# Performance work log

Measured on AMD Instinct MI355X. Metric: run time of the kernel, lower is better.

The kernel has to match this reference:

```python
import jax, jax.numpy as jnp
import numpy as np

V, E, H = 50000, 300, 128
B, L, QL, NS = 64, 1024, 32, 16
ITERATIONS = 3


def _gru_cell(x, h, w_ih, w_hh, b_ih, b_hh):
    # PyTorch GRUCell math.
    gi = x @ w_ih.T + b_ih
    gh = h @ w_hh.T + b_hh
    i_r, i_z, i_n = jnp.split(gi, 3, axis=-1)
    h_r, h_z, h_n = jnp.split(gh, 3, axis=-1)
    r = jax.nn.sigmoid(i_r + h_r)
    z = jax.nn.sigmoid(i_z + h_z)
    n = jnp.tanh(i_n + r * h_n)
    return (1.0 - z) * n + z * h


def _gru_scan(x, w_ih, w_hh, b_ih, b_hh):
    # x: [B, T, E] -> all hidden states [B, T, H] (nn.GRU, batch_first, h0=0).
    gi = jnp.einsum('bte,ge->btg', x, w_ih) + b_ih  # precompute input gates
    hdim = w_hh.shape[1]

    def step(h, gi_t):
        gh = h @ w_hh.T + b_hh
        i_r, i_z, i_n = jnp.split(gi_t, 3, axis=-1)
        h_r, h_z, h_n = jnp.split(gh, 3, axis=-1)
        r = jax.nn.sigmoid(i_r + h_r)
        z = jax.nn.sigmoid(i_z + h_z)
        n = jnp.tanh(i_n + r * h_n)
        h = (1.0 - z) * n + z * h
        return h, h

    h0 = jnp.zeros((x.shape[0], hdim), x.dtype)
    _, hs = jax.lax.scan(step, h0, jnp.swapaxes(gi, 0, 1))
    return jnp.swapaxes(hs, 0, 1)


def setup_inputs() -> dict:
    key = jax.random.key(0)
    ks = jax.random.split(key, 16)
    x_stories = jax.random.randint(ks[0], (B, L), 1, V)
    # Exactly NS sentence-end marks per story (evenly spaced) -> equal sent counts.
    pos = jnp.arange(1, NS + 1) * (L // NS) - 1
    x_story_masks = jnp.zeros((B, L), bool).at[:, pos].set(True)
    x_questions = jax.random.randint(ks[1], (B, QL), 1, V)
    emb = jax.random.normal(ks[2], (V, E), jnp.float32) * 0.1
    s = float(1.0 / np.sqrt(H))
    u = lambda k, sh: jax.random.uniform(k, sh, jnp.float32, -s, s)
    return {
        'x_stories': x_stories,
        'x_story_masks': x_story_masks,
        'x_questions': x_questions,
        'n_sents': NS,
        'emb': emb,
        'enc_w_ih': u(ks[3], (3 * H, E)),
        'enc_w_hh': u(ks[4], (3 * H, H)),
        'enc_b_ih': u(ks[5], (3 * H,)),
        'enc_b_hh': u(ks[6], (3 * H,)),
        'gate_w': u(ks[7], (1, 4 * H)),
        'gate_b': u(ks[8], (1,)),
        'ep_w_ih': u(ks[9], (3 * H, H)),
        'ep_w_hh': u(ks[10], (3 * H, H)),
        'ep_b_ih': u(ks[11], (3 * H,)),
        'ep_b_hh': u(ks[12], (3 * H,)),
    }


def reference(x_stories, x_story_masks, x_questions, n_sents, emb,
              enc_w_ih, enc_w_hh, enc_b_ih, enc_b_hh,
              gate_w, gate_b, ep_w_ih, ep_w_hh, ep_b_ih, ep_b_hh):
    Bb, Ll = x_stories.shape
    enc_stories = _gru_scan(emb[x_stories], enc_w_ih, enc_w_hh, enc_b_ih, enc_b_hh)  # [B,L,H]
    # Gather the n_sents masked (sentence-end) hidden states per story, in order.
    ar = jnp.arange(Ll)
    sort_key = jnp.where(x_story_masks, ar, Ll + ar)
    idx = jnp.argsort(sort_key, axis=1)[:, :n_sents]  # [B,NS]
    sents = jnp.take_along_axis(enc_stories, idx[:, :, None], axis=1)  # [B,NS,H]
    # Question encoding; pick hidden at the last token before padding.
    q_enc = _gru_scan(emb[x_questions], enc_w_ih, enc_w_hh, enc_b_ih, enc_b_hh)
    next_zero = jnp.concatenate([x_questions[:, 1:] == 0, jnp.ones((Bb, 1), bool)], axis=1)
    qi = jnp.argmax(next_zero, axis=1)
    q_vecs = q_enc[jnp.arange(Bb), qi]  # [B,H]
    q = q_vecs[:, None, :]
    pw1 = sents * q
    d1 = (sents - q) ** 2
    mem = q
    hdim = ep_w_hh.shape[1]
    for _ in range(ITERATIONS):
        pw2 = sents * mem
        d2 = (sents - mem) ** 2
        feats = jnp.concatenate([pw1, pw2, d1, d2], axis=2)  # [B,NS,4H]
        gates = jax.nn.sigmoid(feats @ gate_w.T + gate_b)[..., 0]  # [B,NS]

        def ep_step(h, inp):
            x_t, w_t = inp
            h_new = _gru_cell(x_t, h, ep_w_ih, ep_w_hh, ep_b_ih, ep_b_hh)
            w = w_t[:, None]
            return w * h_new + (1.0 - w) * h, None

        h0 = jnp.zeros((Bb, hdim), sents.dtype)
        ep_state, _ = jax.lax.scan(ep_step, h0, (jnp.swapaxes(sents, 0, 1), gates.T))
        mem = ep_state[:, None, :]
    return q_vecs, ep_state[None], gates
```

## Files before the change

kernel.cpp:

```cpp
#include <hip/hip_runtime.h>
#include <hip/hip_bf16.h>

#define HDIM 128
#define G3 384
#define EDIM 300
#define KP 320
#define ASTRIDE 328
#define BATCH 64
#define LSTO 1024
#define QLEN 32
#define NSENT 16
#define WGB 16
#define HROW 272
#define HBUF (WGB * HROW)

typedef float4 f4;
typedef __attribute__((ext_vector_type(8))) short bf16x8;
typedef __attribute__((ext_vector_type(4))) float f32x4;

__device__ __forceinline__ float sigmf(float x) { return 1.0f / (1.0f + __expf(-x)); }
__device__ __forceinline__ float tanhfast(float x) {
    float e = __expf(-2.0f * x);
    return (1.0f - e) / (1.0f + e);
}
__device__ __forceinline__ float bf2f(unsigned short u) {
    return __uint_as_float(((unsigned)u) << 16);
}
__device__ __forceinline__ unsigned short f2bf_u(float f) {
    union { __hip_bfloat16 b; unsigned short s; } u;
    u.b = __float2bfloat16(f);
    return u.s;
}
__device__ __forceinline__ short f2bf_s(float f) {
    union { __hip_bfloat16 b; short s; } u;
    u.b = __float2bfloat16(f);
    return u.s;
}
__device__ __forceinline__ bf16x8 packrow8(const float* p) {
    bf16x8 v;
#pragma unroll
    for (int i = 0; i < 8; i++) v[i] = f2bf_s(p[i]);
    return v;
}
__device__ __forceinline__ unsigned pack2bf(float a, float b) {
    return ((unsigned)f2bf_u(b) << 16) | (unsigned)f2bf_u(a);
}
__device__ __forceinline__ void barrier_nodrain() {
    asm volatile("" ::: "memory");
    __builtin_amdgcn_s_barrier();
    asm volatile("" ::: "memory");
}
__device__ __forceinline__ void lgkm0() {
    asm volatile("s_waitcnt lgkmcnt(0)" ::: "memory");
    __builtin_amdgcn_sched_barrier(0);
}

__global__ __launch_bounds__(256) void k_w2bf(
    const float* __restrict__ w, __hip_bfloat16* __restrict__ wb, int rows)
{
    int i = blockIdx.x * 256 + threadIdx.x;
    if (i >= rows * KP) return;
    int r = i / KP, k = i - r * KP;
    float v = (k < EDIM) ? w[(size_t)r * EDIM + k] : 0.f;
    wb[i] = __float2bfloat16(v);
}

__global__ __launch_bounds__(512) void k_gi_mfma(
    const int* __restrict__ toks, int nrows,
    const float* __restrict__ emb,
    const __hip_bfloat16* __restrict__ wb, const float* __restrict__ b_ih,
    const float* __restrict__ b_hh,
    __hip_bfloat16* __restrict__ gi)
{
    __shared__ __hip_bfloat16 a_lds[32 * ASTRIDE];
    const int tid = threadIdx.x;
    const int rowbase = blockIdx.x * 32;

    for (int i = tid; i < 32 * KP; i += 512) {
        int r = i / KP, k = i - r * KP;
        int row = rowbase + r;
        float v = 0.f;
        if (k < EDIM) {
            int tok = (row < nrows) ? toks[row] : 0;
            v = emb[(size_t)tok * EDIM + k];
        }
        a_lds[r * ASTRIDE + k] = __float2bfloat16(v);
    }
    __syncthreads();

    const int w8   = tid >> 6;
    const int l    = tid & 63;
    const int coln = l & 15;
    const int kg   = l >> 4;

    int g0 = w8 * 48 + coln, g1 = g0 + 16, g2 = g0 + 32;
    float bias0 = b_ih[g0] + (g0 < 256 ? b_hh[g0] : 0.f);
    float bias1 = b_ih[g1] + (g1 < 256 ? b_hh[g1] : 0.f);
    float bias2 = b_ih[g2] + (g2 < 256 ? b_hh[g2] : 0.f);

    f32x4 acc[2][3];
#pragma unroll
    for (int mt = 0; mt < 2; mt++) {
        acc[mt][0] = f32x4{bias0, bias0, bias0, bias0};
        acc[mt][1] = f32x4{bias1, bias1, bias1, bias1};
        acc[mt][2] = f32x4{bias2, bias2, bias2, bias2};
    }

    const __hip_bfloat16* bbase = wb + (size_t)(w8 * 48 + coln) * KP + kg * 8;
#pragma unroll
    for (int c = 0; c < KP / 32; ++c) {
        bf16x8 A0 = *reinterpret_cast<const bf16x8*>(
            a_lds + (coln) * ASTRIDE + c * 32 + kg * 8);
        bf16x8 A1 = *reinterpret_cast<const bf16x8*>(
            a_lds + (16 + coln) * ASTRIDE + c * 32 + kg * 8);
        bf16x8 B0 = *reinterpret_cast<const bf16x8*>(bbase + 0 * 16 * KP + c * 32);
        bf16x8 B1 = *reinterpret_cast<const bf16x8*>(bbase + 1 * 16 * KP + c * 32);
        bf16x8 B2 = *reinterpret_cast<const bf16x8*>(bbase + 2 * 16 * KP + c * 32);
        acc[0][0] = __builtin_amdgcn_mfma_f32_16x16x32_bf16(A0, B0, acc[0][0], 0, 0, 0);
        acc[1][0] = __builtin_amdgcn_mfma_f32_16x16x32_bf16(A1, B0, acc[1][0], 0, 0, 0);
        acc[0][1] = __builtin_amdgcn_mfma_f32_16x16x32_bf16(A0, B1, acc[0][1], 0, 0, 0);
        acc[1][1] = __builtin_amdgcn_mfma_f32_16x16x32_bf16(A1, B1, acc[1][1], 0, 0, 0);
        acc[0][2] = __builtin_amdgcn_mfma_f32_16x16x32_bf16(A0, B2, acc[0][2], 0, 0, 0);
        acc[1][2] = __builtin_amdgcn_mfma_f32_16x16x32_bf16(A1, B2, acc[1][2], 0, 0, 0);
    }

#pragma unroll
    for (int mt = 0; mt < 2; mt++) {
#pragma unroll
        for (int nt = 0; nt < 3; nt++) {
            int gate = w8 * 48 + nt * 16 + coln;
#pragma unroll
            for (int q = 0; q < 4; q++) {
                int row = rowbase + mt * 16 + kg * 4 + q;
                if (row < nrows)
                    gi[(size_t)row * G3 + gate] = __float2bfloat16(acc[mt][nt][q]);
            }
        }
    }
}

__global__ __launch_bounds__(192) void k_gi_dense(
    const float* __restrict__ x, int nrows,
    const float* __restrict__ w_ih, const float* __restrict__ b_ih,
    const float* __restrict__ b_hh,
    __hip_bfloat16* __restrict__ gi)
{
    __shared__ alignas(16) float a_lds[32 * HDIM];
    int tid = threadIdx.x;
    int rowbase = blockIdx.x * 32;

    for (int i = tid; i < 32 * 32; i += 192) {
        int r = i >> 5, e4 = i & 31;
        int row = rowbase + r;
        f4 v;
        if (row < nrows) v = *reinterpret_cast<const f4*>(x + (size_t)row * HDIM + e4 * 4);
        else { v.x = v.y = v.z = v.w = 0.f; }
        *reinterpret_cast<f4*>(a_lds + r * HDIM + e4 * 4) = v;
    }
    __syncthreads();

    int g0 = tid, g1 = tid + 192;
    const float* w0p = w_ih + (size_t)g0 * HDIM;
    const float* w1p = w_ih + (size_t)g1 * HDIM;
    float bb0 = b_ih[g0] + (g0 < 256 ? b_hh[g0] : 0.f);
    float bb1 = b_ih[g1] + (g1 < 256 ? b_hh[g1] : 0.f);

#pragma unroll
    for (int half = 0; half < 2; half++) {
        float acc0[16], acc1[16];
#pragma unroll
        for (int r = 0; r < 16; r++) { acc0[r] = 0.f; acc1[r] = 0.f; }

        for (int e4 = 0; e4 < 32; ++e4) {
            f4 w0 = *reinterpret_cast<const f4*>(w0p + e4 * 4);
            f4 w1 = *reinterpret_cast<const f4*>(w1p + e4 * 4);
#pragma unroll
            for (int r = 0; r < 16; r++) {
                f4 a = *reinterpret_cast<const f4*>(
                    a_lds + (half * 16 + r) * HDIM + e4 * 4);
                acc0[r] += a.x * w0.x + a.y * w0.y + a.z * w0.z + a.w * w0.w;
                acc1[r] += a.x * w1.x + a.y * w1.y + a.z * w1.z + a.w * w1.w;
            }
        }
#pragma unroll
        for (int r = 0; r < 16; r++) {
            int row = rowbase + half * 16 + r;
            if (row < nrows) {
                gi[(size_t)row * G3 + g0] = __float2bfloat16(acc0[r] + bb0);
                gi[(size_t)row * G3 + g1] = __float2bfloat16(acc1[r] + bb1);
            }
        }
    }
}

#define SCAN_BODY(TT, TPF, RB, WB, C, P)                                       \
  {                                                                            \
    const int t_ = (TT);                                                       \
    bf16x8 H0 = *reinterpret_cast<const bf16x8*>(h_raw + (RB) + rd0);          \
    bf16x8 H1 = *reinterpret_cast<const bf16x8*>(h_raw + (RB) + rd1);          \
    bf16x8 H2 = *reinterpret_cast<const bf16x8*>(h_raw + (RB) + rd2);          \
    bf16x8 H3 = *reinterpret_cast<const bf16x8*>(h_raw + (RB) + rd3);          \
    {                                                                          \
      const int tp_ = (TPF);                                                   \
      const unsigned short* gp =                                               \
          reinterpret_cast<const unsigned short*>(gib + (size_t)tp_ * G3);     \
      cr##P = *reinterpret_cast<const ushort4*>(gp + j0);                      \
      cz##P = *reinterpret_cast<const ushort4*>(gp + 128 + j0);                \
      cn##P = *reinterpret_cast<const ushort4*>(gp + 256 + j0);                \
      if (MODE == 0) cm##P = mask[bb * LSTO + tp_];                            \
      if (MODE == 2) cw##P = gsrc[tp_];                                        \
    }                                                                          \
    f32x4 accr = {bf2f(cr##C.x), bf2f(cr##C.y), bf2f(cr##C.z), bf2f(cr##C.w)};\
    f32x4 accz = {bf2f(cz##C.x), bf2f(cz##C.y), bf2f(cz##C.z), bf2f(cz##C.w)};\
    f32x4 accn = {bn4.x, bn4.y, bn4.z, bn4.w};                                 \
    __builtin_amdgcn_s_setprio(1);                                             \
    accr = __builtin_amdgcn_mfma_f32_16x16x32_bf16(Ar0, H0, accr, 0, 0, 0);    \
    accz = __builtin_amdgcn_mfma_f32_16x16x32_bf16(Az0, H0, accz, 0, 0, 0);    \
    accn = __builtin_amdgcn_mfma_f32_16x16x32_bf16(An0, H0, accn, 0, 0, 0);    \
    accr = __builtin_amdgcn_mfma_f32_16x16x32_bf16(Ar1, H1, accr, 0, 0, 0);    \
    accz = __builtin_amdgcn_mfma_f32_16x16x32_bf16(Az1, H1, accz, 0, 0, 0);    \
    accn = __builtin_amdgcn_mfma_f32_16x16x32_bf16(An1, H1, accn, 0, 0, 0);    \
    accr = __builtin_amdgcn_mfma_f32_16x16x32_bf16(Ar2, H2, accr, 0, 0, 0);    \
    accz = __builtin_amdgcn_mfma_f32_16x16x32_bf16(Az2, H2, accz, 0, 0, 0);    \
    accn = __builtin_amdgcn_mfma_f32_16x16x32_bf16(An2, H2, accn, 0, 0, 0);    \
    accr = __builtin_amdgcn_mfma_f32_16x16x32_bf16(Ar3, H3, accr, 0, 0, 0);    \
    accz = __builtin_amdgcn_mfma_f32_16x16x32_bf16(Az3, H3, accz, 0, 0, 0);    \
    accn = __builtin_amdgcn_mfma_f32_16x16x32_bf16(An3, H3, accn, 0, 0, 0);    \
    __builtin_amdgcn_s_setprio(0);                                             \
    {                                                                          \
      float r0 = sigmf(accr[0]);                                               \
      float r1 = sigmf(accr[1]);                                               \
      float r2 = sigmf(accr[2]);                                               \
      float r3 = sigmf(accr[3]);                                               \
      float z0 = sigmf(accz[0]);                                               \
      float z1 = sigmf(accz[1]);                                               \
      float z2 = sigmf(accz[2]);                                               \
      float z3 = sigmf(accz[3]);                                               \
      float n0 = tanhfast(bf2f(cn##C.x) + r0 * accn[0]);                       \
      float n1 = tanhfast(bf2f(cn##C.y) + r1 * accn[1]);                       \
      float n2 = tanhfast(bf2f(cn##C.z) + r2 * accn[2]);                       \
      float n3 = tanhfast(bf2f(cn##C.w) + r3 * accn[3]);                       \
      float h0 = n0 + z0 * (hp0 - n0);                                         \
      float h1 = n1 + z1 * (hp1 - n1);                                         \
      float h2 = n2 + z2 * (hp2 - n2);                                         \
      float h3 = n3 + z3 * (hp3 - n3);                                         \
      if (MODE == 2) {                                                         \
        h0 = hp0 + cw##C * (h0 - hp0);                                         \
        h1 = hp1 + cw##C * (h1 - hp1);                                         \
        h2 = hp2 + cw##C * (h2 - hp2);                                         \
        h3 = hp3 + cw##C * (h3 - hp3);                                         \
      }                                                                        \
      hp0 = h0; hp1 = h1; hp2 = h2; hp3 = h3;                                  \
    }                                                                          \
    {                                                                          \
      uint2 hw_;                                                               \
      hw_.x = pack2bf(hp0, hp1);                                               \
      hw_.y = pack2bf(hp2, hp3);                                               \
      *reinterpret_cast<uint2*>(h_raw + (WB) + wroff) = hw_;                   \
    }                                                                          \
    if (MODE == 0) {                                                           \
      if (cm##C) {                                                             \
        if (scnt < NSENT) {                                                    \
          float4 v_ = make_float4(hp0, hp1, hp2, hp3);                         \
          *reinterpret_cast<float4*>(                                          \
              sents + ((size_t)bb * NSENT + scnt) * HDIM + j0) = v_;           \
        }                                                                      \
        scnt++;                                                                \
      }                                                                        \
    }                                                                          \
    if (MODE == 1 && t_ == qi) {                                               \
      float4 v_ = make_float4(hp0, hp1, hp2, hp3);                             \
      *reinterpret_cast<float4*>(qv_out + bb * HDIM + j0) = v_;                \
      *reinterpret_cast<float4*>(q_ws + bb * HDIM + j0) = v_;                  \
    }                                                                          \
    if (MODE == 2 && t_ == T - 1) {                                            \
      float4 v_ = make_float4(hp0, hp1, hp2, hp3);                             \
      *reinterpret_cast<float4*>(mem_lds + col * HDIM + j0) = v_;              \
      if (ep_out)                                                              \
        *reinterpret_cast<float4*>(ep_out + bb * HDIM + j0) = v_;              \
    }                                                                          \
    lgkm0();                                                                   \
    barrier_nodrain();                                                         \
  }

template <int MODE>
__device__ __forceinline__ void scan_core(
    const __hip_bfloat16* __restrict__ gi, int T,
    const float* __restrict__ w_hh, const float* __restrict__ b_hh,
    const int* __restrict__ mask, float* __restrict__ sents,
    const int* __restrict__ qtoks, float* __restrict__ qv_out,
    float* __restrict__ q_ws,
    const float* __restrict__ gl_lds,
    float* __restrict__ ep_out,
    float* __restrict__ mem_lds,
    int b0, unsigned char* __restrict__ h_raw)
{
    const int tid = threadIdx.x;
    const int w   = tid >> 6;
    const int l   = tid & 63;
    const int col = l & 15;
    const int kg  = l >> 4;
    const int bb  = b0 + col;
    const int j0  = 16 * w + 4 * kg;

    const float* wr = w_hh + (size_t)(16 * w + col) * HDIM + kg * 8;
    const float* wz = w_hh + (size_t)(128 + 16 * w + col) * HDIM + kg * 8;
    const float* wn = w_hh + (size_t)(256 + 16 * w + col) * HDIM + kg * 8;
    bf16x8 Ar0 = packrow8(wr +  0), Ar1 = packrow8(wr + 32),
           Ar2 = packrow8(wr + 64), Ar3 = packrow8(wr + 96);
    bf16x8 Az0 = packrow8(wz +  0), Az1 = packrow8(wz + 32),
           Az2 = packrow8(wz + 64), Az3 = packrow8(wz + 96);
    bf16x8 An0 = packrow8(wn +  0), An1 = packrow8(wn + 32),
           An2 = packrow8(wn + 64), An3 = packrow8(wn + 96);
    asm volatile("" : "+v"(Ar0), "+v"(Ar1), "+v"(Ar2), "+v"(Ar3));
    asm volatile("" : "+v"(Az0), "+v"(Az1), "+v"(Az2), "+v"(Az3));
    asm volatile("" : "+v"(An0), "+v"(An1), "+v"(An2), "+v"(An3));

    f4 bn4 = *reinterpret_cast<const f4*>(b_hh + 256 + j0);
    const float* gsrc = (MODE == 2) ? (gl_lds + col * NSENT) : nullptr;

    const int rd0 = col * HROW + 0 * 64 + kg * 16;
    const int rd1 = col * HROW + 1 * 64 + kg * 16;
    const int rd2 = col * HROW + 2 * 64 + kg * 16;
    const int rd3 = col * HROW + 3 * 64 + kg * 16;
    const int wroff = col * HROW + j0 * 2;

    for (int i = tid; i < 2 * HBUF / 4; i += 512)
        reinterpret_cast<unsigned*>(h_raw)[i] = 0u;

    int qi = QLEN - 1;
    if (MODE == 1) {
        for (int t2 = 0; t2 < QLEN - 1; t2++)
            if (qtoks[bb * QLEN + t2 + 1] == 0) { qi = t2; break; }
    }
    int scnt = 0;

    const __hip_bfloat16* gib = gi + (size_t)bb * T * G3;
    ushort4 crA, czA, cnA, crB, czB, cnB;
    int cmA = 0, cmB = 0;
    float cwA = 0.f, cwB = 0.f;
    __syncthreads();
    {
        const unsigned short* gp = reinterpret_cast<const unsigned short*>(gib);
        crA = *reinterpret_cast<const ushort4*>(gp + j0);
        czA = *reinterpret_cast<const ushort4*>(gp + 128 + j0);
        cnA = *reinterpret_cast<const ushort4*>(gp + 256 + j0);
        if (MODE == 0) cmA = mask[bb * LSTO];
        if (MODE == 2) cwA = gsrc[0];
    }
    float hp0 = 0.f, hp1 = 0.f, hp2 = 0.f, hp3 = 0.f;
    __syncthreads();

    for (int t = 0; t < T; t += 2) {
        SCAN_BODY(t,     t + 1,                       0,    HBUF, A, B)
        SCAN_BODY(t + 1, (t + 2 < T ? t + 2 : t + 1), HBUF, 0,    B, A)
    }
}

__global__ __launch_bounds__(512, 1) void k_scan01(
    const __hip_bfloat16* __restrict__ gi_sto,
    const __hip_bfloat16* __restrict__ gi_q,
    const float* __restrict__ w_hh, const float* __restrict__ b_hh,
    const int* __restrict__ mask, float* __restrict__ sents,
    const int* __restrict__ qtoks, float* __restrict__ qv_out,
    float* __restrict__ q_ws)
{
    __shared__ alignas(16) unsigned char h_raw[2 * HBUF];
    if (blockIdx.x < 4) {
        scan_core<0>(gi_sto, LSTO, w_hh, b_hh, mask, sents,
                     nullptr, nullptr, nullptr, nullptr, nullptr, nullptr,
                     blockIdx.x * WGB, h_raw);
    } else {
        scan_core<1>(gi_q, QLEN, w_hh, b_hh, nullptr, nullptr,
                     qtoks, qv_out, q_ws, nullptr, nullptr, nullptr,
                     (blockIdx.x - 4) * WGB, h_raw);
    }
}

__global__ __launch_bounds__(512, 1) void k_ep(
    const __hip_bfloat16* __restrict__ gi_ep,
    const float* __restrict__ w_hh, const float* __restrict__ b_hh,
    const float* __restrict__ sents, const float* __restrict__ q_ws,
    const float* __restrict__ gate_w, const float* __restrict__ gate_b,
    float* __restrict__ out_g, float* __restrict__ out_ep)
{
    __shared__ alignas(16) unsigned char h_raw[2 * HBUF];
    __shared__ float gl[WGB * NSENT];
    __shared__ alignas(16) float mem_lds[WGB * HDIM];

    const int tid = threadIdx.x;
    const int b0 = blockIdx.x * WGB;
    const float gb0 = gate_b[0];

    for (int it = 0; it < 3; ++it) {
        if (tid < 256) {
            int bq = tid >> 4, tq = tid & 15;
            int b = b0 + bq;
            const float* sv = sents + ((size_t)b * NSENT + tq) * HDIM;
            const float* Qv = q_ws + (size_t)b * HDIM;
            const float* Mv = mem_lds + bq * HDIM;
            float p = 0.f;
            for (int j = 0; j < HDIM; j++) {
                float S = sv[j], Q = Qv[j];
                float M = (it == 0) ? Q : Mv[j];
                float dq = S - Q, dm = S - M;
                p += (S * Q) * gate_w[j] + (S * M) * gate_w[HDIM + j] +
                     (dq * dq) * gate_w[2 * HDIM + j] +
                     (dm * dm) * gate_w[3 * HDIM + j];
            }
            float g = sigmf(p + gb0);
            gl[bq * NSENT + tq] = g;
            if (it == 2) out_g[b * NSENT + tq] = g;
        }
        scan_core<2>(gi_ep, NSENT, w_hh, b_hh, nullptr, nullptr,
                     nullptr, nullptr, nullptr, gl,
                     (it == 2) ? out_ep : nullptr, mem_lds,
                     b0, h_raw);
        __syncthreads();
    }
}

extern "C" void kernel_launch(void* const* d_in, const int* in_sizes, int n_in,
                              void* d_out, int out_size, void* d_ws, size_t ws_size,
                              hipStream_t stream)
{
    const int*   x_sto    = (const int*)d_in[0];
    const int*   x_mask   = (const int*)d_in[1];
    const int*   x_q      = (const int*)d_in[2];
    const float* emb      = (const float*)d_in[4];
    const float* enc_w_ih = (const float*)d_in[5];
    const float* enc_w_hh = (const float*)d_in[6];
    const float* enc_b_ih = (const float*)d_in[7];
    const float* enc_b_hh = (const float*)d_in[8];
    const float* gate_w   = (const float*)d_in[9];
    const float* gate_b   = (const float*)d_in[10];
    const float* ep_w_ih  = (const float*)d_in[11];
    const float* ep_w_hh  = (const float*)d_in[12];
    const float* ep_b_ih  = (const float*)d_in[13];
    const float* ep_b_hh  = (const float*)d_in[14];

    float* out_q  = (float*)d_out;
    float* out_ep = (float*)d_out + BATCH * HDIM;
    float* out_g  = (float*)d_out + 2 * BATCH * HDIM;

    char* ws = (char*)d_ws;
    size_t off = 0;
    auto alloc = [&](size_t bytes) {
        void* p = ws + off;
        off += (bytes + 255) & ~(size_t)255;
        return p;
    };
    __hip_bfloat16* gi_sto = (__hip_bfloat16*)alloc((size_t)BATCH * LSTO * G3 * 2);
    __hip_bfloat16* gi_q   = (__hip_bfloat16*)alloc((size_t)BATCH * QLEN * G3 * 2);
    __hip_bfloat16* gi_ep  = (__hip_bfloat16*)alloc((size_t)BATCH * NSENT * G3 * 2);
    __hip_bfloat16* wb_enc = (__hip_bfloat16*)alloc((size_t)G3 * KP * 2);
    float* sents    = (float*)alloc((size_t)BATCH * NSENT * HDIM * 4);
    float* q_ws     = (float*)alloc((size_t)BATCH * HDIM * 4);
    (void)ws_size; (void)in_sizes; (void)n_in; (void)out_size;

    k_w2bf<<<(G3 * KP + 255) / 256, 256, 0, stream>>>(enc_w_ih, wb_enc, G3);

    k_gi_mfma<<<(BATCH * LSTO) / 32, 512, 0, stream>>>(
        x_sto, BATCH * LSTO, emb, wb_enc, enc_b_ih, enc_b_hh, gi_sto);
    k_gi_mfma<<<(BATCH * QLEN) / 32, 512, 0, stream>>>(
        x_q, BATCH * QLEN, emb, wb_enc, enc_b_ih, enc_b_hh, gi_q);

    k_scan01<<<8, 512, 0, stream>>>(
        gi_sto, gi_q, enc_w_hh, enc_b_hh, x_mask, sents, x_q, out_q, q_ws);

    k_gi_dense<<<(BATCH * NSENT) / 32, 192, 0, stream>>>(
        sents, BATCH * NSENT, ep_w_ih, ep_b_ih, ep_b_hh, gi_ep);
    k_ep<<<BATCH / WGB, 512, 0, stream>>>(
        gi_ep, ep_w_hh, ep_b_hh, sents, q_ws, gate_w, gate_b, out_g, out_ep);
}
```

Measured before the change: 1.307 ms.

## Prescale gate preactivations for exp2 activations, merge gi launches, vectorize loads

```diff
diff --git a/kernel.cpp b/kernel.cpp
--- a/kernel.cpp
+++ b/kernel.cpp
@@ -14,15 +14,29 @@
 #define HROW 272
 #define HBUF (WGB * HROW)
 
+#define S2F (-1.44269504088896340736f)
+#define SNF (-2.88539008177792681472f)
+
 typedef float4 f4;
 typedef __attribute__((ext_vector_type(8))) short bf16x8;
 typedef __attribute__((ext_vector_type(4))) float f32x4;
 
-__device__ __forceinline__ float sigmf(float x) { return 1.0f / (1.0f + __expf(-x)); }
-__device__ __forceinline__ float tanhfast(float x) {
-    float e = __expf(-2.0f * x);
-    return (1.0f - e) / (1.0f + e);
-}
+#if __has_builtin(__builtin_amdgcn_exp2f)
+__device__ __forceinline__ float exp2_f(float x) { return __builtin_amdgcn_exp2f(x); }
+#else
+__device__ __forceinline__ float exp2_f(float x) { return exp2f(x); }
+#endif
+#if __has_builtin(__builtin_amdgcn_rcpf)
+__device__ __forceinline__ float rcp_f(float x) { return __builtin_amdgcn_rcpf(x); }
+#else
+__device__ __forceinline__ float rcp_f(float x) { return 1.0f / x; }
+#endif
+
+__device__ __forceinline__ float sigm2(float b) { return rcp_f(1.0f + exp2_f(b)); }
+__device__ __forceinline__ float tanh2(float c) {
+    return __builtin_fmaf(2.0f, rcp_f(1.0f + exp2_f(c)), -1.0f);
+}
+
 __device__ __forceinline__ float bf2f(unsigned short u) {
     return __uint_as_float(((unsigned)u) << 16);
 }
@@ -36,10 +50,10 @@
     u.b = __float2bfloat16(f);
     return u.s;
 }
-__device__ __forceinline__ bf16x8 packrow8(const float* p) {
+__device__ __forceinline__ bf16x8 packrow8s(const float* p, float s) {
     bf16x8 v;
 #pragma unroll
-    for (int i = 0; i < 8; i++) v[i] = f2bf_s(p[i]);
+    for (int i = 0; i < 8; i++) v[i] = f2bf_s(p[i] * s);
     return v;
 }
 __device__ __forceinline__ unsigned pack2bf(float a, float b) {
@@ -66,25 +80,37 @@
 }
 
 __global__ __launch_bounds__(512) void k_gi_mfma(
-    const int* __restrict__ toks, int nrows,
+    const int* __restrict__ toks_a, int nrows_a, __hip_bfloat16* __restrict__ gi_a,
+    const int* __restrict__ toks_b, int nrows_b, __hip_bfloat16* __restrict__ gi_b,
     const float* __restrict__ emb,
     const __hip_bfloat16* __restrict__ wb, const float* __restrict__ b_ih,
-    const float* __restrict__ b_hh,
-    __hip_bfloat16* __restrict__ gi)
+    const float* __restrict__ b_hh)
 {
     __shared__ __hip_bfloat16 a_lds[32 * ASTRIDE];
     const int tid = threadIdx.x;
-    const int rowbase = blockIdx.x * 32;
-
-    for (int i = tid; i < 32 * KP; i += 512) {
-        int r = i / KP, k = i - r * KP;
+    const int nb_a = nrows_a / 32;
+
+    const int* toks;
+    int nrows, rowbase;
+    __hip_bfloat16* gi;
+    if ((int)blockIdx.x < nb_a) {
+        toks = toks_a; nrows = nrows_a; rowbase = blockIdx.x * 32; gi = gi_a;
+    } else {
+        toks = toks_b; nrows = nrows_b; rowbase = (blockIdx.x - nb_a) * 32; gi = gi_b;
+    }
+
+    for (int i = tid; i < 32 * (KP / 4); i += 512) {
+        int r = i / (KP / 4), k4 = (i - r * (KP / 4)) * 4;
         int row = rowbase + r;
-        float v = 0.f;
-        if (k < EDIM) {
+        f4 v = make_float4(0.f, 0.f, 0.f, 0.f);
+        if (k4 < EDIM) {
             int tok = (row < nrows) ? toks[row] : 0;
-            v = emb[(size_t)tok * EDIM + k];
+            v = *reinterpret_cast<const f4*>(emb + (size_t)tok * EDIM + k4);
         }
-        a_lds[r * ASTRIDE + k] = __float2bfloat16(v);
+        uint2 pk;
+        pk.x = pack2bf(v.x, v.y);
+        pk.y = pack2bf(v.z, v.w);
+        *reinterpret_cast<uint2*>(a_lds + r * ASTRIDE + k4) = pk;
     }
     __syncthreads();
 
@@ -129,11 +155,13 @@
 #pragma unroll
         for (int nt = 0; nt < 3; nt++) {
             int gate = w8 * 48 + nt * 16 + coln;
+            float sc = (gate < 256) ? S2F : SNF;
 #pragma unroll
             for (int q = 0; q < 4; q++) {
                 int row = rowbase + mt * 16 + kg * 4 + q;
                 if (row < nrows)
-                    gi[(size_t)row * G3 + gate] = __float2bfloat16(acc[mt][nt][q]);
+                    gi[(size_t)row * G3 + gate] =
+                        __float2bfloat16(acc[mt][nt][q] * sc);
             }
         }
     }
@@ -164,6 +192,8 @@
     const float* w1p = w_ih + (size_t)g1 * HDIM;
     float bb0 = b_ih[g0] + (g0 < 256 ? b_hh[g0] : 0.f);
     float bb1 = b_ih[g1] + (g1 < 256 ? b_hh[g1] : 0.f);
+    float s0 = (g0 < 256) ? S2F : SNF;
+    float s1 = (g1 < 256) ? S2F : SNF;
 
 #pragma unroll
     for (int half = 0; half < 2; half++) {
@@ -186,8 +216,8 @@
         for (int r = 0; r < 16; r++) {
             int row = rowbase + half * 16 + r;
             if (row < nrows) {
-                gi[(size_t)row * G3 + g0] = __float2bfloat16(acc0[r] + bb0);
-                gi[(size_t)row * G3 + g1] = __float2bfloat16(acc1[r] + bb1);
+                gi[(size_t)row * G3 + g0] = __float2bfloat16((acc0[r] + bb0) * s0);
+                gi[(size_t)row * G3 + g1] = __float2bfloat16((acc1[r] + bb1) * s1);
             }
         }
     }
@@ -228,18 +258,18 @@
     accn = __builtin_amdgcn_mfma_f32_16x16x32_bf16(An3, H3, accn, 0, 0, 0);    \
     __builtin_amdgcn_s_setprio(0);                                             \
     {                                                                          \
-      float r0 = sigmf(accr[0]);                                               \
-      float r1 = sigmf(accr[1]);                                               \
-      float r2 = sigmf(accr[2]);                                               \
-      float r3 = sigmf(accr[3]);                                               \
-      float z0 = sigmf(accz[0]);                                               \
-      float z1 = sigmf(accz[1]);                                               \
-      float z2 = sigmf(accz[2]);                                               \
-      float z3 = sigmf(accz[3]);                                               \
-      float n0 = tanhfast(bf2f(cn##C.x) + r0 * accn[0]);                       \
-      float n1 = tanhfast(bf2f(cn##C.y) + r1 * accn[1]);                       \
-      float n2 = tanhfast(bf2f(cn##C.z) + r2 * accn[2]);                       \
-      float n3 = tanhfast(bf2f(cn##C.w) + r3 * accn[3]);                       \
+      float r0 = sigm2(accr[0]);                                               \
+      float r1 = sigm2(accr[1]);                                               \
+      float r2 = sigm2(accr[2]);                                               \
+      float r3 = sigm2(accr[3]);                                               \
+      float z0 = sigm2(accz[0]);                                               \
+      float z1 = sigm2(accz[1]);                                               \
+      float z2 = sigm2(accz[2]);                                               \
+      float z3 = sigm2(accz[3]);                                               \
+      float n0 = tanh2(bf2f(cn##C.x) + r0 * accn[0]);                          \
+      float n1 = tanh2(bf2f(cn##C.y) + r1 * accn[1]);                          \
+      float n2 = tanh2(bf2f(cn##C.z) + r2 * accn[2]);                          \
+      float n3 = tanh2(bf2f(cn##C.w) + r3 * accn[3]);                          \
       float h0 = n0 + z0 * (hp0 - n0);                                         \
       float h1 = n1 + z1 * (hp1 - n1);                                         \
       float h2 = n2 + z2 * (hp2 - n2);                                         \
@@ -306,17 +336,18 @@
     const float* wr = w_hh + (size_t)(16 * w + col) * HDIM + kg * 8;
     const float* wz = w_hh + (size_t)(128 + 16 * w + col) * HDIM + kg * 8;
     const float* wn = w_hh + (size_t)(256 + 16 * w + col) * HDIM + kg * 8;
-    bf16x8 Ar0 = packrow8(wr +  0), Ar1 = packrow8(wr + 32),
-           Ar2 = packrow8(wr + 64), Ar3 = packrow8(wr + 96);
-    bf16x8 Az0 = packrow8(wz +  0), Az1 = packrow8(wz + 32),
-           Az2 = packrow8(wz + 64), Az3 = packrow8(wz + 96);
-    bf16x8 An0 = packrow8(wn +  0), An1 = packrow8(wn + 32),
-           An2 = packrow8(wn + 64), An3 = packrow8(wn + 96);
+    bf16x8 Ar0 = packrow8s(wr +  0, S2F), Ar1 = packrow8s(wr + 32, S2F),
+           Ar2 = packrow8s(wr + 64, S2F), Ar3 = packrow8s(wr + 96, S2F);
+    bf16x8 Az0 = packrow8s(wz +  0, S2F), Az1 = packrow8s(wz + 32, S2F),
+           Az2 = packrow8s(wz + 64, S2F), Az3 = packrow8s(wz + 96, S2F);
+    bf16x8 An0 = packrow8s(wn +  0, SNF), An1 = packrow8s(wn + 32, SNF),
+           An2 = packrow8s(wn + 64, SNF), An3 = packrow8s(wn + 96, SNF);
     asm volatile("" : "+v"(Ar0), "+v"(Ar1), "+v"(Ar2), "+v"(Ar3));
     asm volatile("" : "+v"(Az0), "+v"(Az1), "+v"(Az2), "+v"(Az3));
     asm volatile("" : "+v"(An0), "+v"(An1), "+v"(An2), "+v"(An3));
 
-    f4 bn4 = *reinterpret_cast<const f4*>(b_hh + 256 + j0);
+    f4 bnl = *reinterpret_cast<const f4*>(b_hh + 256 + j0);
+    f4 bn4 = make_float4(bnl.x * SNF, bnl.y * SNF, bnl.z * SNF, bnl.w * SNF);
     const float* gsrc = (MODE == 2) ? (gl_lds + col * NSENT) : nullptr;
 
     const int rd0 = col * HROW + 0 * 64 + kg * 16;
@@ -400,15 +431,28 @@
             const float* Qv = q_ws + (size_t)b * HDIM;
             const float* Mv = mem_lds + bq * HDIM;
             float p = 0.f;
-            for (int j = 0; j < HDIM; j++) {
-                float S = sv[j], Q = Qv[j];
-                float M = (it == 0) ? Q : Mv[j];
-                float dq = S - Q, dm = S - M;
-                p += (S * Q) * gate_w[j] + (S * M) * gate_w[HDIM + j] +
-                     (dq * dq) * gate_w[2 * HDIM + j] +
-                     (dm * dm) * gate_w[3 * HDIM + j];
+            for (int j4 = 0; j4 < HDIM / 4; j4++) {
+                f4 S = *reinterpret_cast<const f4*>(sv + j4 * 4);
+                f4 Q = *reinterpret_cast<const f4*>(Qv + j4 * 4);
+                f4 M;
+                if (it == 0) M = Q;
+                else M = *reinterpret_cast<const f4*>(Mv + j4 * 4);
+                f4 w0 = *reinterpret_cast<const f4*>(gate_w + j4 * 4);
+                f4 w1 = *reinterpret_cast<const f4*>(gate_w + HDIM + j4 * 4);
+                f4 w2 = *reinterpret_cast<const f4*>(gate_w + 2 * HDIM + j4 * 4);
+                f4 w3 = *reinterpret_cast<const f4*>(gate_w + 3 * HDIM + j4 * 4);
+                float dqx = S.x - Q.x, dqy = S.y - Q.y, dqz = S.z - Q.z, dqw = S.w - Q.w;
+                float dmx = S.x - M.x, dmy = S.y - M.y, dmz = S.z - M.z, dmw = S.w - M.w;
+                p += (S.x * Q.x) * w0.x + (S.y * Q.y) * w0.y +
+                     (S.z * Q.z) * w0.z + (S.w * Q.w) * w0.w;
+                p += (S.x * M.x) * w1.x + (S.y * M.y) * w1.y +
+                     (S.z * M.z) * w1.z + (S.w * M.w) * w1.w;
+                p += (dqx * dqx) * w2.x + (dqy * dqy) * w2.y +
+                     (dqz * dqz) * w2.z + (dqw * dqw) * w2.w;
+                p += (dmx * dmx) * w3.x + (dmy * dmy) * w3.y +
+                     (dmz * dmz) * w3.z + (dmw * dmw) * w3.w;
             }
-            float g = sigmf(p + gb0);
+            float g = sigm2(S2F * (p + gb0));
             gl[bq * NSENT + tq] = g;
             if (it == 2) out_g[b * NSENT + tq] = g;
         }
@@ -460,10 +504,9 @@
 
     k_w2bf<<<(G3 * KP + 255) / 256, 256, 0, stream>>>(enc_w_ih, wb_enc, G3);
 
-    k_gi_mfma<<<(BATCH * LSTO) / 32, 512, 0, stream>>>(
-        x_sto, BATCH * LSTO, emb, wb_enc, enc_b_ih, enc_b_hh, gi_sto);
-    k_gi_mfma<<<(BATCH * QLEN) / 32, 512, 0, stream>>>(
-        x_q, BATCH * QLEN, emb, wb_enc, enc_b_ih, enc_b_hh, gi_q);
+    k_gi_mfma<<<(BATCH * LSTO) / 32 + (BATCH * QLEN) / 32, 512, 0, stream>>>(
+        x_sto, BATCH * LSTO, gi_sto, x_q, BATCH * QLEN, gi_q,
+        emb, wb_enc, enc_b_ih, enc_b_hh);
 
     k_scan01<<<8, 512, 0, stream>>>(
         gi_sto, gi_q, enc_w_hh, enc_b_hh, x_mask, sents, x_q, out_q, q_ws);
```

Result: faster. 1.110 ms (-15.1%).
